# Kernel optimization log

Measured on AMD Instinct MI355X. Metric: run time of the kernel, lower is better.

Reference implementation:

```python
import jax, jax.numpy as jnp
import numpy as np

# OGB/PyG molecular featurization vocab sizes (x_map / e_map)
NODE_VOCABS = [119, 9, 11, 12, 10, 5, 8, 2, 2]   # 9 atom features
EDGE_VOCABS = [22, 6, 2]                          # 3 bond features
HID, OUT, LAYERS = 128, 256, 3
N_NODES, N_EDGES, N_GRAPHS = 200000, 400000, 8000
NODE_OFF = np.concatenate([[0], np.cumsum(NODE_VOCABS)[:-1]]).astype(np.int32)
EDGE_OFF = np.concatenate([[0], np.cumsum(EDGE_VOCABS)[:-1]]).astype(np.int32)
NODE_TOT = int(np.sum(NODE_VOCABS))
EDGE_TOT = int(np.sum(EDGE_VOCABS))


def setup_inputs() -> dict:
    key = jax.random.key(0)
    ks = jax.random.split(key, 16)
    # integer graph data (values in-range per categorical column via modulo)
    x = jax.random.randint(ks[0], (N_NODES, 9), 0, 1 << 30) % jnp.asarray(NODE_VOCABS)
    edge_attr = jax.random.randint(ks[1], (N_EDGES, 3), 0, 1 << 30) % jnp.asarray(EDGE_VOCABS)
    edge_index = jax.random.randint(ks[2], (2, N_EDGES), 0, N_NODES)
    batch = jnp.sort(jax.random.randint(ks[3], (N_NODES,), 0, N_GRAPHS))
    s = 0.02
    return {
        "x": x, "edge_attr": edge_attr, "edge_index": edge_index, "batch": batch,
        # embedding tables packed row-wise with per-feature offsets
        "node_emb": jax.random.normal(ks[4], (NODE_TOT, HID), jnp.float32) * s,
        "edge_emb": jax.random.normal(ks[5], (EDGE_TOT, HID), jnp.float32) * s,
        "node_proj_w": jax.random.normal(ks[6], (9 * HID, HID), jnp.float32) * s,
        "node_proj_b": jnp.zeros((HID,), jnp.float32),
        "edge_proj_w": jax.random.normal(ks[7], (3 * HID, HID), jnp.float32) * s,
        "edge_proj_b": jnp.zeros((HID,), jnp.float32),
        "mlp_w1": jax.random.normal(ks[8], (LAYERS, HID, HID), jnp.float32) * s,
        "mlp_b1": jnp.zeros((LAYERS, HID), jnp.float32),
        "mlp_w2": jax.random.normal(ks[9], (LAYERS, HID, HID), jnp.float32) * s,
        "mlp_b2": jnp.zeros((LAYERS, HID), jnp.float32),
        "proj_w": jax.random.normal(ks[10], (HID, OUT), jnp.float32) * s,
        "proj_b": jnp.zeros((OUT,), jnp.float32),
    }


def reference(x, edge_attr, edge_index, batch,
              node_emb, edge_emb,
              node_proj_w, node_proj_b, edge_proj_w, edge_proj_b,
              mlp_w1, mlp_b1, mlp_w2, mlp_b2, proj_w, proj_b):
    n = x.shape[0]
    e = edge_attr.shape[0]
    # embedding lookup per categorical column, concat, project -> [N, HID]
    nf = node_emb[x + jnp.asarray(NODE_OFF)].reshape(n, 9 * HID)
    h = nf @ node_proj_w + node_proj_b
    ef = edge_emb[edge_attr + jnp.asarray(EDGE_OFF)].reshape(e, 3 * HID)
    ef = ef @ edge_proj_w + edge_proj_b
    src, dst = edge_index[0], edge_index[1]
    for l in range(LAYERS):
        # GINEConv (eps=0): mlp(x + sum_{j->i} relu(x_j + e_ji)), then outer relu
        m = jax.nn.relu(h[src] + ef)                       # [E, HID] gather + fuse
        agg = jax.ops.segment_sum(m, dst, num_segments=N_NODES)
        z = h + agg
        z = jax.nn.relu(z @ mlp_w1[l] + mlp_b1[l]) @ mlp_w2[l] + mlp_b2[l]
        h = jax.nn.relu(z)
    g = jax.ops.segment_sum(h, batch, num_segments=N_GRAPHS)  # global_add_pool
    p = g @ proj_w + proj_b
    norm = jnp.maximum(jnp.linalg.norm(p, axis=-1, keepdims=True), 1e-12)
    return p / norm
```

## Files before the change

### kernel.cpp

```cpp
#include <hip/hip_runtime.h>
#include <hip/hip_bf16.h>

#define NN 200000
#define NE 400000
#define NG 8000
#define HID 128
#define OUTD 256
#define NODE_TOT 178
#define EDGE_TOT 30
#define NCOMBO 264
#define SCAN_NB 196

typedef __attribute__((ext_vector_type(8))) short bfrag8;
typedef __attribute__((ext_vector_type(4))) short bfrag4;
typedef __attribute__((ext_vector_type(4))) float f32x4;
typedef unsigned short ushort_t;

__constant__ int c_noff[10] = {0,119,128,139,151,161,166,174,176,178};

__device__ __forceinline__ ushort_t f2bf(float f) {
  union { float f; unsigned u; } x; x.f = f;
  unsigned r = x.u + 0x7fffu + ((x.u >> 16) & 1u);
  return (ushort_t)(r >> 16);
}
__device__ __forceinline__ float bf2f(ushort_t u) {
  union { unsigned u; float f; } x; x.u = ((unsigned)u) << 16;
  return x.f;
}

__global__ __launch_bounds__(128) void build_tables(
    const float* __restrict__ node_emb, const float* __restrict__ edge_emb,
    const float* __restrict__ npw, const float* __restrict__ npb,
    const float* __restrict__ epw, const float* __restrict__ epb,
    float* __restrict__ PN, float* __restrict__ PE)
{
  int r = blockIdx.x, d = threadIdx.x;
  if (r < NODE_TOT) {
    int c = 0;
    while (r >= c_noff[c+1]) c++;
    float acc = (c == 0) ? npb[d] : 0.f;
    const float* er = node_emb + r*HID;
    const float* wb = npw + (size_t)(c*HID)*HID + d;
    for (int k = 0; k < HID; k++) acc += er[k] * wb[(size_t)k*HID];
    PN[r*HID + d] = acc;
  } else {
    int re = r - NODE_TOT;
    int c = (re >= 28) ? 2 : (re >= 22 ? 1 : 0);
    float acc = (c == 0) ? epb[d] : 0.f;
    const float* er = edge_emb + re*HID;
    const float* wb = epw + (size_t)(c*HID)*HID + d;
    for (int k = 0; k < HID; k++) acc += er[k] * wb[(size_t)k*HID];
    PE[re*HID + d] = acc;
  }
}

__global__ __launch_bounds__(64) void build_pe3(const float* __restrict__ PE,
                                                unsigned* __restrict__ pe3b)
{
  int c = blockIdx.x, lane = threadIdx.x;
  int a2 = c & 1, a1 = (c >> 1) % 6, a0 = (c >> 1) / 6;
  int d = lane*2;
  float v0 = PE[a0*HID + d]   + PE[(22+a1)*HID + d]   + PE[(28+a2)*HID + d];
  float v1 = PE[a0*HID + d+1] + PE[(22+a1)*HID + d+1] + PE[(28+a2)*HID + d+1];
  pe3b[c*64 + lane] = (unsigned)f2bf(v0) | ((unsigned)f2bf(v1) << 16);
}

__global__ __launch_bounds__(256) void pack_w1(const float* __restrict__ w1,
                                               ushort_t* __restrict__ pw)
{
  int t = blockIdx.x*256 + threadIdx.x;
  int lane = t & 63, tile = (t >> 6) & 31, layer = t >> 11;
  int nt = tile >> 2, kt = tile & 3;
  int n  = nt*16 + (lane & 15);
  int k0 = kt*32 + ((lane >> 4) << 3);
  const float* src = w1 + (size_t)layer*HID*HID;
  ushort_t* dst = pw + (size_t)layer*32768 + (size_t)tile*512 + lane*8;
  #pragma unroll
  for (int j = 0; j < 8; j++) dst[j] = f2bf(src[(size_t)(k0+j)*HID + n]);
}

__global__ __launch_bounds__(256) void pack_w2(const float* __restrict__ w2,
                                               ushort_t* __restrict__ pw)
{
  int t = blockIdx.x*256 + threadIdx.x;
  int lane = t & 63, frag = (t >> 6) & 63, layer = t >> 12;
  int it = frag >> 3, kk = frag & 7;
  int i  = it*16 + (lane & 15);
  int k0 = kk*16 + ((lane >> 4) << 2);
  const float* src = w2 + (size_t)layer*HID*HID;
  ushort_t* dst = pw + (size_t)layer*32768 + 16384 + (size_t)frag*256 + lane*4;
  #pragma unroll
  for (int j = 0; j < 4; j++) dst[j] = f2bf(src[(size_t)(k0+j)*HID + i]);
}

__global__ __launch_bounds__(256) void node_embed(const int* __restrict__ x,
                                                  const float* __restrict__ PN,
                                                  ushort_t* __restrict__ h)
{
  int gid = blockIdx.x*256 + threadIdx.x;
  int i = gid >> 5, d0 = (gid & 31) << 2;
  const int* xr = x + i*9;
  f32x4 acc = {0.f, 0.f, 0.f, 0.f};
  #pragma unroll
  for (int c = 0; c < 9; c++)
    acc += *(const f32x4*)&PN[(c_noff[c] + xr[c])*HID + d0];
  uint2 pk;
  pk.x = (unsigned)f2bf(acc[0]) | ((unsigned)f2bf(acc[1]) << 16);
  pk.y = (unsigned)f2bf(acc[2]) | ((unsigned)f2bf(acc[3]) << 16);
  *(uint2*)&h[(size_t)i*HID + d0] = pk;
}

__global__ __launch_bounds__(256) void hist(const int* __restrict__ ei, int* __restrict__ deg) {
  int e = blockIdx.x*256 + threadIdx.x;
  if (e < NE) atomicAdd(&deg[ei[NE + e]], 1);
}

__global__ __launch_bounds__(256) void scan1(const int* __restrict__ deg,
                                             int* __restrict__ rowptr,
                                             int* __restrict__ bsum)
{
  __shared__ int sd[256];
  int b = blockIdx.x, t = threadIdx.x;
  int idx0 = b*1024 + t*4;
  int v[4]; int s = 0;
  #pragma unroll
  for (int j = 0; j < 4; j++) { int i = idx0 + j; v[j] = (i < NN) ? deg[i] : 0; s += v[j]; }
  sd[t] = s; __syncthreads();
  for (int off = 1; off < 256; off <<= 1) {
    int x = (t >= off) ? sd[t - off] : 0; __syncthreads();
    sd[t] += x; __syncthreads();
  }
  int run = (t > 0) ? sd[t-1] : 0;
  #pragma unroll
  for (int j = 0; j < 4; j++) { int i = idx0 + j; run += v[j]; if (i < NN) rowptr[i+1] = run; }
  if (t == 255) bsum[b] = sd[255];
}

__global__ __launch_bounds__(256) void scan2(int* __restrict__ bsum) {
  __shared__ int sd[256];
  int t = threadIdx.x;
  sd[t] = (t < SCAN_NB) ? bsum[t] : 0; __syncthreads();
  for (int off = 1; off < 256; off <<= 1) {
    int x = (t >= off) ? sd[t - off] : 0; __syncthreads();
    sd[t] += x; __syncthreads();
  }
  if (t < SCAN_NB) bsum[t] = sd[t];
}

__global__ __launch_bounds__(256) void scan3(int* __restrict__ rowptr, const int* __restrict__ bsum) {
  int b = blockIdx.x, t = threadIdx.x;
  if (b == 0) { if (t == 0) rowptr[0] = 0; return; }
  int add = bsum[b-1];
  int idx0 = b*1024 + t*4;
  #pragma unroll
  for (int j = 0; j < 4; j++) { int i = idx0 + j; if (i < NN) rowptr[i+1] += add; }
}

__global__ __launch_bounds__(256) void scatter_e(const int* __restrict__ ei,
                                                 const int* __restrict__ ea,
                                                 int* __restrict__ cursor,
                                                 unsigned* __restrict__ elist,
                                                 unsigned char* __restrict__ dloc)
{
  int e = blockIdx.x*256 + threadIdx.x;
  if (e >= NE) return;
  int src = ei[e], dst = ei[NE + e];
  const int* ar = ea + e*3;
  unsigned combo = (unsigned)((ar[0]*6 + ar[1])*2 + ar[2]);
  int pos = atomicAdd(&cursor[dst], 1);
  elist[pos] = (unsigned)src | (combo << 18);
  dloc[pos] = (unsigned char)(dst & 63);
}

template<bool LAST>
__global__ __launch_bounds__(256, 4) void gine_layer(
    const ushort_t* __restrict__ hin, ushort_t* __restrict__ hout,
    const int* __restrict__ rowptr, const unsigned* __restrict__ elist,
    const unsigned char* __restrict__ dloc,
    const unsigned* __restrict__ pe3b,
    const ushort_t* __restrict__ pw,
    const float* __restrict__ b1, const float* __restrict__ b2,
    const int* __restrict__ batch, float* __restrict__ gf)
{
  __shared__ ushort_t aggs[64*136];
  __shared__ int bids[64];
  int tid = threadIdx.x;
  int w = tid >> 6, lane = tid & 63;
  int q = lane >> 4;
  int rb = blockIdx.x*64 + w*16;
  const unsigned* h2 = (const unsigned*)hin;

  if (LAST && tid < 64) bids[tid] = batch[blockIdx.x*64 + tid];

  #pragma unroll
  for (int r = 0; r < 16; r++)
    ((unsigned*)&aggs[(w*16 + r)*136])[lane] = 0;

  int s = rowptr[rb], E = rowptr[rb + 16];
  int cur = -1;
  float ax = 0.f, ay = 0.f;

  auto proc = [&](int dl, unsigned hv, unsigned tt) {
    int dlu = __builtin_amdgcn_readfirstlane(dl);
    if (dlu != cur) {
      if (cur >= 0)
        ((unsigned*)&aggs[cur*136])[lane] =
            (unsigned)f2bf(ax) | ((unsigned)f2bf(ay) << 16);
      cur = dlu; ax = 0.f; ay = 0.f;
    }
    ax += fmaxf(bf2f((ushort_t)(hv & 0xffff)) + bf2f((ushort_t)(tt & 0xffff)), 0.f);
    ay += fmaxf(bf2f((ushort_t)(hv >> 16)) + bf2f((ushort_t)(tt >> 16)), 0.f);
  };

  int j = s;
  for (; j + 7 < E; j += 8) {
    unsigned pk[8]; int dl[8]; unsigned hv[8], tt[8];
    #pragma unroll
    for (int k = 0; k < 8; k++) { pk[k] = elist[j+k]; dl[k] = dloc[j+k]; }
    #pragma unroll
    for (int k = 0; k < 8; k++) {
      hv[k] = h2[(size_t)(pk[k] & 0x3ffff)*64 + lane];
      tt[k] = pe3b[(pk[k] >> 18)*64 + lane];
    }
    #pragma unroll
    for (int k = 0; k < 8; k++) proc(dl[k], hv[k], tt[k]);
  }
  for (; j < E; ++j) {
    unsigned pk = elist[j];
    int dl = dloc[j];
    unsigned hv = h2[(size_t)(pk & 0x3ffff)*64 + lane];
    unsigned tt = pe3b[(pk >> 18)*64 + lane];
    proc(dl, hv, tt);
  }
  if (cur >= 0)
    ((unsigned*)&aggs[cur*136])[lane] =
        (unsigned)f2bf(ax) | ((unsigned)f2bf(ay) << 16);

  int n = rb + (lane & 15);
  int acol = q << 3;

  bfrag8 afr[4];
  #pragma unroll
  for (int kt = 0; kt < 4; kt++) {
    int c = kt*32 + acol;
    bfrag8 hfr = *(const bfrag8*)(hin + (size_t)n*HID + c);
    bfrag8 gfr = *(const bfrag8*)&aggs[(w*16 + (lane & 15))*136 + c];
    bfrag8 fr;
    #pragma unroll
    for (int j2 = 0; j2 < 8; j2++)
      fr[j2] = (short)f2bf(bf2f((ushort_t)hfr[j2]) + bf2f((ushort_t)gfr[j2]));
    afr[kt] = fr;
  }

  if (LAST) __syncthreads();

  const bfrag8* w1f = (const bfrag8*)pw;
  const bfrag4* w2f = (const bfrag4*)(pw + 16384);

  f32x4 acc1[8];
  #pragma unroll
  for (int nt = 0; nt < 8; nt++)
    acc1[nt] = *(const f32x4*)&b1[nt*16 + q*4];
  #pragma unroll
  for (int kt = 0; kt < 4; kt++)
    #pragma unroll
    for (int nt = 0; nt < 8; nt++)
      acc1[nt] = __builtin_amdgcn_mfma_f32_16x16x32_bf16(w1f[(nt*4+kt)*64 + lane], afr[kt], acc1[nt], 0, 0, 0);

  bfrag4 t4[8];
  #pragma unroll
  for (int kk = 0; kk < 8; kk++) {
    bfrag4 v;
    #pragma unroll
    for (int r = 0; r < 4; r++) v[r] = (short)f2bf(fmaxf(acc1[kk][r], 0.f));
    t4[kk] = v;
  }

  #pragma unroll
  for (int it = 0; it < 8; it++) {
    f32x4 acc2 = *(const f32x4*)&b2[it*16 + q*4];
    #pragma unroll
    for (int kk = 0; kk < 8; kk++)
      acc2 = __builtin_amdgcn_mfma_f32_16x16x16bf16_1k(w2f[(it*8+kk)*64 + lane], t4[kk], acc2, 0, 0, 0);
    uint2 pk;
    pk.x = (unsigned)f2bf(fmaxf(acc2[0], 0.f)) | ((unsigned)f2bf(fmaxf(acc2[1], 0.f)) << 16);
    pk.y = (unsigned)f2bf(fmaxf(acc2[2], 0.f)) | ((unsigned)f2bf(fmaxf(acc2[3], 0.f)) << 16);
    if (LAST) {
      *(uint2*)&aggs[(w*16 + (lane & 15))*136 + it*16 + q*4] = pk;
    } else {
      *(uint2*)&hout[(size_t)n*HID + it*16 + q*4] = pk;
    }
  }

  if (LAST) {
    __syncthreads();
    int d = tid & 127, rh = tid >> 7;
    float acc = 0.f;
    int curg = bids[rh*32];
    for (int r = 0; r < 32; r++) {
      int row = rh*32 + r;
      int g = bids[row];
      if (g != curg) {
        atomicAdd(&gf[(size_t)curg*HID + d], acc);
        acc = 0.f; curg = g;
      }
      acc += bf2f(aggs[row*136 + d]);
    }
    atomicAdd(&gf[(size_t)curg*HID + d], acc);
  }
}

__global__ __launch_bounds__(256) void final_proj(const float* __restrict__ gf,
                                                  const float* __restrict__ W,
                                                  const float* __restrict__ b,
                                                  float* __restrict__ out)
{
  __shared__ float gls[16*128];
  __shared__ float part[16][4];
  int tid = threadIdx.x;
  int gbase = blockIdx.x*16;
  for (int idx = tid; idx < 2048; idx += 256) gls[idx] = gf[(size_t)gbase*128 + idx];
  __syncthreads();
  float acc[16];
  #pragma unroll
  for (int g = 0; g < 16; g++) acc[g] = 0.f;
  for (int k = 0; k < 128; k++) {
    float wv = W[(size_t)k*256 + tid];
    #pragma unroll
    for (int g = 0; g < 16; g++) acc[g] += gls[g*128 + k] * wv;
  }
  float bj = b[tid];
  int wid = tid >> 6, lane = tid & 63;
  #pragma unroll
  for (int g = 0; g < 16; g++) {
    acc[g] += bj;
    float s = acc[g]*acc[g];
    #pragma unroll
    for (int off = 32; off > 0; off >>= 1) s += __shfl_xor(s, off, 64);
    if (lane == 0) part[g][wid] = s;
  }
  __syncthreads();
  #pragma unroll
  for (int g = 0; g < 16; g++) {
    float S = part[g][0] + part[g][1] + part[g][2] + part[g][3];
    float rn = 1.f / fmaxf(sqrtf(S), 1e-12f);
    out[(size_t)(gbase + g)*256 + tid] = acc[g]*rn;
  }
}

__global__ __launch_bounds__(256) void ws_diag(float* __restrict__ out, int n, float wsval) {
  int i = blockIdx.x*256 + threadIdx.x;
  if (i < n) out[i] = (i == 0) ? wsval : 0.f;
}

extern "C" void kernel_launch(void* const* d_in, const int* in_sizes, int n_in,
                              void* d_out, int out_size, void* d_ws, size_t ws_size,
                              hipStream_t stream)
{
  const int*   x     = (const int*)d_in[0];
  const int*   ea    = (const int*)d_in[1];
  const int*   ei    = (const int*)d_in[2];
  const int*   batch = (const int*)d_in[3];
  const float* nemb  = (const float*)d_in[4];
  const float* eemb  = (const float*)d_in[5];
  const float* npw   = (const float*)d_in[6];
  const float* npb   = (const float*)d_in[7];
  const float* epw   = (const float*)d_in[8];
  const float* epb   = (const float*)d_in[9];
  const float* w1    = (const float*)d_in[10];
  const float* b1    = (const float*)d_in[11];
  const float* w2    = (const float*)d_in[12];
  const float* b2    = (const float*)d_in[13];
  const float* pjw   = (const float*)d_in[14];
  const float* pjb   = (const float*)d_in[15];
  float* out = (float*)d_out;

  char* ws = (char*)d_ws;
  size_t off = 0;
  auto carve = [&](size_t bytes) -> char* {
    char* p = ws + off;
    off = (off + bytes + 255) & ~(size_t)255;
    return p;
  };
  float*    PN     = (float*)carve((size_t)NODE_TOT*HID*4);
  float*    PE     = (float*)carve((size_t)EDGE_TOT*HID*4);
  unsigned* PE3b   = (unsigned*)carve((size_t)NCOMBO*64*4);
  ushort_t* PW     = (ushort_t*)carve((size_t)3*32768*2);
  ushort_t* hA     = (ushort_t*)carve((size_t)NN*HID*2);
  ushort_t* hB     = (ushort_t*)carve((size_t)NN*HID*2);
  float*    gf     = (float*)carve((size_t)NG*HID*4);
  int*      deg    = (int*)carve((size_t)NN*4);
  int*      rowptr = (int*)carve((size_t)(NN+1)*4);
  int*      cursor = (int*)carve((size_t)NN*4);
  int*      bsum   = (int*)carve((size_t)SCAN_NB*4);
  unsigned* elist  = (unsigned*)carve((size_t)NE*4);
  unsigned char* dlc = (unsigned char*)carve((size_t)NE);

  if (off > ws_size) {
    ws_diag<<<(out_size + 255)/256, 256, 0, stream>>>(out, out_size, (float)ws_size);
    return;
  }

  build_tables<<<NODE_TOT + EDGE_TOT, 128, 0, stream>>>(nemb, eemb, npw, npb, epw, epb, PN, PE);
  build_pe3<<<NCOMBO, 64, 0, stream>>>(PE, PE3b);
  pack_w1<<<24, 256, 0, stream>>>(w1, PW);
  pack_w2<<<48, 256, 0, stream>>>(w2, PW);
  node_embed<<<(NN*32)/256, 256, 0, stream>>>(x, PN, hA);

  hipMemsetAsync(deg, 0, (size_t)NN*4, stream);
  hipMemsetAsync(gf, 0, (size_t)NG*HID*4, stream);
  hist<<<(NE + 255)/256, 256, 0, stream>>>(ei, deg);
  scan1<<<SCAN_NB, 256, 0, stream>>>(deg, rowptr, bsum);
  scan2<<<1, 256, 0, stream>>>(bsum);
  scan3<<<SCAN_NB, 256, 0, stream>>>(rowptr, bsum);
  hipMemcpyAsync(cursor, rowptr, (size_t)NN*4, hipMemcpyDeviceToDevice, stream);
  scatter_e<<<(NE + 255)/256, 256, 0, stream>>>(ei, ea, cursor, elist, dlc);

  gine_layer<false><<<NN/64, 256, 0, stream>>>(hA, hB, rowptr, elist, dlc, PE3b,
                                               PW, b1, b2, batch, gf);
  gine_layer<false><<<NN/64, 256, 0, stream>>>(hB, hA, rowptr, elist, dlc, PE3b,
                                               PW + 32768, b1 + HID, b2 + HID, batch, gf);
  gine_layer<true><<<NN/64, 256, 0, stream>>>(hA, hB, rowptr, elist, dlc, PE3b,
                                              PW + 65536, b1 + 2*HID, b2 + 2*HID, batch, gf);

  final_proj<<<NG/16, 256, 0, stream>>>(gf, pjw, pjb, out);
}
```

Before: 447.9 us.

## Merge setup kernels, fold cursor copy into scan, widen edge-gather unroll

```diff
diff --git a/kernel.cpp b/kernel.cpp
--- a/kernel.cpp
+++ b/kernel.cpp
@@ -7,7 +7,6 @@
 #define HID 128
 #define OUTD 256
 #define NODE_TOT 178
-#define EDGE_TOT 30
 #define NCOMBO 264
 #define SCAN_NB 196
 
@@ -28,14 +27,17 @@
   return x.f;
 }
 
-__global__ __launch_bounds__(128) void build_tables(
+__global__ __launch_bounds__(128) void setup_tables(
     const float* __restrict__ node_emb, const float* __restrict__ edge_emb,
     const float* __restrict__ npw, const float* __restrict__ npb,
     const float* __restrict__ epw, const float* __restrict__ epb,
-    float* __restrict__ PN, float* __restrict__ PE)
-{
-  int r = blockIdx.x, d = threadIdx.x;
-  if (r < NODE_TOT) {
+    const float* __restrict__ w1, const float* __restrict__ w2,
+    float* __restrict__ PN, unsigned* __restrict__ pe3b,
+    ushort_t* __restrict__ pw)
+{
+  int b = blockIdx.x, tid = threadIdx.x;
+  if (b < NODE_TOT) {
+    int r = b, d = tid;
     int c = 0;
     while (r >= c_noff[c+1]) c++;
     float acc = (c == 0) ? npb[d] : 0.f;
@@ -43,54 +45,46 @@
     const float* wb = npw + (size_t)(c*HID)*HID + d;
     for (int k = 0; k < HID; k++) acc += er[k] * wb[(size_t)k*HID];
     PN[r*HID + d] = acc;
+  } else if (b < NODE_TOT + NCOMBO) {
+    if (tid >= 64) return;
+    int c = b - NODE_TOT, lane = tid;
+    int a2 = c & 1, a1 = (c >> 1) % 6, a0 = (c >> 1) / 6;
+    int row[3] = { a0, 22 + a1, 28 + a2 };
+    float v0 = epb[lane*2], v1 = epb[lane*2 + 1];
+    #pragma unroll
+    for (int f = 0; f < 3; f++) {
+      const float* er = edge_emb + row[f]*HID;
+      const float* wb = epw + (size_t)(f*HID)*HID;
+      for (int k = 0; k < HID; k++) {
+        float e = er[k];
+        v0 += e * wb[(size_t)k*HID + lane*2];
+        v1 += e * wb[(size_t)k*HID + lane*2 + 1];
+      }
+    }
+    pe3b[c*64 + lane] = (unsigned)f2bf(v0) | ((unsigned)f2bf(v1) << 16);
   } else {
-    int re = r - NODE_TOT;
-    int c = (re >= 28) ? 2 : (re >= 22 ? 1 : 0);
-    float acc = (c == 0) ? epb[d] : 0.f;
-    const float* er = edge_emb + re*HID;
-    const float* wb = epw + (size_t)(c*HID)*HID + d;
-    for (int k = 0; k < HID; k++) acc += er[k] * wb[(size_t)k*HID];
-    PE[re*HID + d] = acc;
-  }
-}
-
-__global__ __launch_bounds__(64) void build_pe3(const float* __restrict__ PE,
-                                                unsigned* __restrict__ pe3b)
-{
-  int c = blockIdx.x, lane = threadIdx.x;
-  int a2 = c & 1, a1 = (c >> 1) % 6, a0 = (c >> 1) / 6;
-  int d = lane*2;
-  float v0 = PE[a0*HID + d]   + PE[(22+a1)*HID + d]   + PE[(28+a2)*HID + d];
-  float v1 = PE[a0*HID + d+1] + PE[(22+a1)*HID + d+1] + PE[(28+a2)*HID + d+1];
-  pe3b[c*64 + lane] = (unsigned)f2bf(v0) | ((unsigned)f2bf(v1) << 16);
-}
-
-__global__ __launch_bounds__(256) void pack_w1(const float* __restrict__ w1,
-                                               ushort_t* __restrict__ pw)
-{
-  int t = blockIdx.x*256 + threadIdx.x;
-  int lane = t & 63, tile = (t >> 6) & 31, layer = t >> 11;
-  int nt = tile >> 2, kt = tile & 3;
-  int n  = nt*16 + (lane & 15);
-  int k0 = kt*32 + ((lane >> 4) << 3);
-  const float* src = w1 + (size_t)layer*HID*HID;
-  ushort_t* dst = pw + (size_t)layer*32768 + (size_t)tile*512 + lane*8;
-  #pragma unroll
-  for (int j = 0; j < 8; j++) dst[j] = f2bf(src[(size_t)(k0+j)*HID + n]);
-}
-
-__global__ __launch_bounds__(256) void pack_w2(const float* __restrict__ w2,
-                                               ushort_t* __restrict__ pw)
-{
-  int t = blockIdx.x*256 + threadIdx.x;
-  int lane = t & 63, frag = (t >> 6) & 63, layer = t >> 12;
-  int it = frag >> 3, kk = frag & 7;
-  int i  = it*16 + (lane & 15);
-  int k0 = kk*16 + ((lane >> 4) << 2);
-  const float* src = w2 + (size_t)layer*HID*HID;
-  ushort_t* dst = pw + (size_t)layer*32768 + 16384 + (size_t)frag*256 + lane*4;
-  #pragma unroll
-  for (int j = 0; j < 4; j++) dst[j] = f2bf(src[(size_t)(k0+j)*HID + i]);
+    int t = (b - NODE_TOT - NCOMBO)*128 + tid;
+    if (t < 6144) {
+      int lane = t & 63, tile = (t >> 6) & 31, layer = t >> 11;
+      int nt = tile >> 2, kt = tile & 3;
+      int n  = nt*16 + (lane & 15);
+      int k0 = kt*32 + ((lane >> 4) << 3);
+      const float* src = w1 + (size_t)layer*HID*HID;
+      ushort_t* dst = pw + (size_t)layer*32768 + (size_t)tile*512 + lane*8;
+      #pragma unroll
+      for (int j = 0; j < 8; j++) dst[j] = f2bf(src[(size_t)(k0+j)*HID + n]);
+    } else {
+      int t2 = t - 6144;
+      int lane = t2 & 63, frag = (t2 >> 6) & 63, layer = t2 >> 12;
+      int it = frag >> 3, kk = frag & 7;
+      int i  = it*16 + (lane & 15);
+      int k0 = kk*16 + ((lane >> 4) << 2);
+      const float* src = w2 + (size_t)layer*HID*HID;
+      ushort_t* dst = pw + (size_t)layer*32768 + 16384 + (size_t)frag*256 + lane*4;
+      #pragma unroll
+      for (int j = 0; j < 4; j++) dst[j] = f2bf(src[(size_t)(k0+j)*HID + i]);
+    }
+  }
 }
 
 __global__ __launch_bounds__(256) void node_embed(const int* __restrict__ x,
@@ -147,20 +141,30 @@
   if (t < SCAN_NB) bsum[t] = sd[t];
 }
 
-__global__ __launch_bounds__(256) void scan3(int* __restrict__ rowptr, const int* __restrict__ bsum) {
+__global__ __launch_bounds__(256) void scan3(int* __restrict__ rowptr,
+                                             const int* __restrict__ bsum,
+                                             int* __restrict__ cursor)
+{
   int b = blockIdx.x, t = threadIdx.x;
-  if (b == 0) { if (t == 0) rowptr[0] = 0; return; }
-  int add = bsum[b-1];
+  int add = (b > 0) ? bsum[b-1] : 0;
+  if (b == 0 && t == 0) { rowptr[0] = 0; cursor[0] = 0; }
   int idx0 = b*1024 + t*4;
   #pragma unroll
-  for (int j = 0; j < 4; j++) { int i = idx0 + j; if (i < NN) rowptr[i+1] += add; }
+  for (int j = 0; j < 4; j++) {
+    int i = idx0 + j;
+    if (i < NN) {
+      int v = rowptr[i+1] + add;
+      rowptr[i+1] = v;
+      cursor[i+1] = v;
+    }
+  }
 }
 
 __global__ __launch_bounds__(256) void scatter_e(const int* __restrict__ ei,
                                                  const int* __restrict__ ea,
                                                  int* __restrict__ cursor,
                                                  unsigned* __restrict__ elist,
-                                                 unsigned char* __restrict__ dloc)
+                                                 int* __restrict__ dloc)
 {
   int e = blockIdx.x*256 + threadIdx.x;
   if (e >= NE) return;
@@ -169,14 +173,14 @@
   unsigned combo = (unsigned)((ar[0]*6 + ar[1])*2 + ar[2]);
   int pos = atomicAdd(&cursor[dst], 1);
   elist[pos] = (unsigned)src | (combo << 18);
-  dloc[pos] = (unsigned char)(dst & 63);
+  dloc[pos] = dst & 63;
 }
 
 template<bool LAST>
 __global__ __launch_bounds__(256, 4) void gine_layer(
     const ushort_t* __restrict__ hin, ushort_t* __restrict__ hout,
     const int* __restrict__ rowptr, const unsigned* __restrict__ elist,
-    const unsigned char* __restrict__ dloc,
+    const int* __restrict__ dloc,
     const unsigned* __restrict__ pe3b,
     const ushort_t* __restrict__ pw,
     const float* __restrict__ b1, const float* __restrict__ b2,
@@ -196,7 +200,8 @@
   for (int r = 0; r < 16; r++)
     ((unsigned*)&aggs[(w*16 + r)*136])[lane] = 0;
 
-  int s = rowptr[rb], E = rowptr[rb + 16];
+  int s = __builtin_amdgcn_readfirstlane(rowptr[rb]);
+  int E = __builtin_amdgcn_readfirstlane(rowptr[rb + 16]);
   int cur = -1;
   float ax = 0.f, ay = 0.f;
 
@@ -213,17 +218,17 @@
   };
 
   int j = s;
-  for (; j + 7 < E; j += 8) {
-    unsigned pk[8]; int dl[8]; unsigned hv[8], tt[8];
-    #pragma unroll
-    for (int k = 0; k < 8; k++) { pk[k] = elist[j+k]; dl[k] = dloc[j+k]; }
-    #pragma unroll
-    for (int k = 0; k < 8; k++) {
+  for (; j + 11 < E; j += 12) {
+    unsigned pk[12]; int dl[12]; unsigned hv[12], tt[12];
+    #pragma unroll
+    for (int k = 0; k < 12; k++) { pk[k] = elist[j+k]; dl[k] = dloc[j+k]; }
+    #pragma unroll
+    for (int k = 0; k < 12; k++) {
       hv[k] = h2[(size_t)(pk[k] & 0x3ffff)*64 + lane];
       tt[k] = pe3b[(pk[k] >> 18)*64 + lane];
     }
     #pragma unroll
-    for (int k = 0; k < 8; k++) proc(dl[k], hv[k], tt[k]);
+    for (int k = 0; k < 12; k++) proc(dl[k], hv[k], tt[k]);
   }
   for (; j < E; ++j) {
     unsigned pk = elist[j];
@@ -383,37 +388,32 @@
     return p;
   };
   float*    PN     = (float*)carve((size_t)NODE_TOT*HID*4);
-  float*    PE     = (float*)carve((size_t)EDGE_TOT*HID*4);
   unsigned* PE3b   = (unsigned*)carve((size_t)NCOMBO*64*4);
   ushort_t* PW     = (ushort_t*)carve((size_t)3*32768*2);
   ushort_t* hA     = (ushort_t*)carve((size_t)NN*HID*2);
   ushort_t* hB     = (ushort_t*)carve((size_t)NN*HID*2);
+  int*      deg    = (int*)carve((size_t)NN*4);
   float*    gf     = (float*)carve((size_t)NG*HID*4);
-  int*      deg    = (int*)carve((size_t)NN*4);
   int*      rowptr = (int*)carve((size_t)(NN+1)*4);
-  int*      cursor = (int*)carve((size_t)NN*4);
+  int*      cursor = (int*)carve((size_t)(NN+1)*4);
   int*      bsum   = (int*)carve((size_t)SCAN_NB*4);
   unsigned* elist  = (unsigned*)carve((size_t)NE*4);
-  unsigned char* dlc = (unsigned char*)carve((size_t)NE);
+  int*      dlc    = (int*)carve((size_t)NE*4);
 
   if (off > ws_size) {
     ws_diag<<<(out_size + 255)/256, 256, 0, stream>>>(out, out_size, (float)ws_size);
     return;
   }
 
-  build_tables<<<NODE_TOT + EDGE_TOT, 128, 0, stream>>>(nemb, eemb, npw, npb, epw, epb, PN, PE);
-  build_pe3<<<NCOMBO, 64, 0, stream>>>(PE, PE3b);
-  pack_w1<<<24, 256, 0, stream>>>(w1, PW);
-  pack_w2<<<48, 256, 0, stream>>>(w2, PW);
+  setup_tables<<<NODE_TOT + NCOMBO + 144, 128, 0, stream>>>(
+      nemb, eemb, npw, npb, epw, epb, w1, w2, PN, PE3b, PW);
   node_embed<<<(NN*32)/256, 256, 0, stream>>>(x, PN, hA);
 
-  hipMemsetAsync(deg, 0, (size_t)NN*4, stream);
-  hipMemsetAsync(gf, 0, (size_t)NG*HID*4, stream);
+  hipMemsetAsync(deg, 0, (size_t)NN*4 + (size_t)NG*HID*4, stream);
   hist<<<(NE + 255)/256, 256, 0, stream>>>(ei, deg);
   scan1<<<SCAN_NB, 256, 0, stream>>>(deg, rowptr, bsum);
   scan2<<<1, 256, 0, stream>>>(bsum);
-  scan3<<<SCAN_NB, 256, 0, stream>>>(rowptr, bsum);
-  hipMemcpyAsync(cursor, rowptr, (size_t)NN*4, hipMemcpyDeviceToDevice, stream);
+  scan3<<<SCAN_NB, 256, 0, stream>>>(rowptr, bsum, cursor);
   scatter_e<<<(NE + 255)/256, 256, 0, stream>>>(ei, ea, cursor, elist, dlc);
 
   gine_layer<false><<<NN/64, 256, 0, stream>>>(hA, hB, rowptr, elist, dlc, PE3b,
```

New measurement: 446.4 us. No clear change (-0.3%).
